# Performance work log

Measured on AMD Instinct MI355X. Metric: run time of the kernel, lower is better.

Reference implementation:

```python
import jax, jax.numpy as jnp
import numpy as np

M, B, N, D, DFF, DCOND = 8, 8, 2048, 512, 2048, 512


def setup_inputs() -> dict:
    key = jax.random.key(0)
    ks = jax.random.split(key, 8)
    s = 0.02  # weight init scale
    return {
        "x": jax.random.normal(ks[0], (B, N, D), dtype=jnp.float32),
        "cond": jax.random.normal(ks[1], (B, DCOND), dtype=jnp.float32),
        "route": jax.random.randint(ks[2], (B,), 0, M, dtype=jnp.int64),
        "W_cond": jax.random.normal(ks[3], (M, DCOND, 2 * D), dtype=jnp.float32) * s,
        "b_cond": jnp.zeros((M, 2 * D), dtype=jnp.float32),
        "W1": jax.random.normal(ks[4], (M, D, DFF), dtype=jnp.float32) * s,
        "b1": jnp.zeros((M, DFF), dtype=jnp.float32),
        "W2": jax.random.normal(ks[5], (M, DFF, D), dtype=jnp.float32) * s,
        "b2": jnp.zeros((M, D), dtype=jnp.float32),
    }


def reference(x, cond, route, W_cond, b_cond, W1, b1, W2, b2):
    # --- all branches computed densely (faithful to the torch module) ---
    # cond modulation per branch: [M, B, 2D]
    mod = jnp.einsum('bc,mcd->mbd', cond, W_cond) + b_cond[:, None, :]
    scale, shift = jnp.split(mod, 2, axis=-1)            # each [M, B, D]
    # FiLM modulate tokens: [M, B, N, D]
    x_mod = x[None] * (1.0 + scale[:, :, None, :]) + shift[:, :, None, :]
    # MLP per branch
    h = jax.nn.gelu(jnp.einsum('mbnd,mdf->mbnf', x_mod, W1) + b1[:, None, None, :])
    stacked = jnp.einsum('mbnf,mfd->mbnd', h, W2) + b2[:, None, None, :]  # [M,B,N,D]
    # --- one-hot select (torch.einsum('mbnd,bm->bnd', stacked, one_hot)) ---
    one_hot = jax.nn.one_hot(route, M, dtype=stacked.dtype)  # [B, M]
    return jnp.einsum('mbnd,bm->bnd', stacked, one_hot)
```

## Files before the change

### kernel.cpp

```cpp
#include <hip/hip_runtime.h>
#include <hip/hip_bf16.h>
#include <cstdint>
#include <cstddef>

#define NEXP   8
#define BATCH  8
#define NTOK   2048
#define DDIM   512
#define DFFDIM 2048
#define DCOND  512

typedef float  f32x4  __attribute__((ext_vector_type(4)));
typedef __bf16 bf16x8 __attribute__((ext_vector_type(8)));

using as1_cvoid = __attribute__((address_space(1))) const void;
using as3_void  = __attribute__((address_space(3))) void;

__device__ __forceinline__ void async_copy16(const void* g, void* l) {
  __builtin_amdgcn_global_load_lds((as1_cvoid*)g, (as3_void*)l, 16, 0, 0);
}

__device__ __forceinline__ unsigned short f2bf_bits(float f) {
  __hip_bfloat16 h = __float2bfloat16(f);
  return *reinterpret_cast<unsigned short*>(&h);
}

__device__ __forceinline__ float gelu_fast(float v) {
  float y = v * fmaf(0.0713548162726f, v * v, 1.5957691216057f);
  float e = exp2f(-1.44269504089f * y);
  return v * __builtin_amdgcn_rcpf(1.0f + e);
}

__global__ void mod_kernel(const float* __restrict__ cond,
                           const int* __restrict__ route,
                           const float* __restrict__ W_cond,
                           const float* __restrict__ b_cond,
                           float* __restrict__ ss) {
  const int b = blockIdx.y;
  const int m = route[b];
  const int tj = threadIdx.x & 63;
  const int cq = threadIdx.x >> 6;
  const int j = blockIdx.x * 64 + tj;
  const float* wc = W_cond + (size_t)m * DCOND * (2 * DDIM);
  const float* cb = cond + (size_t)b * DCOND;
  float acc = 0.f;
#pragma unroll 4
  for (int c = cq * 128; c < cq * 128 + 128; ++c)
    acc += cb[c] * wc[(size_t)c * (2 * DDIM) + j];
  __shared__ float red[4][64];
  red[cq][tj] = acc;
  __syncthreads();
  if (cq == 0) {
    float v = red[0][tj] + red[1][tj] + red[2][tj] + red[3][tj];
    ss[(size_t)b * (2 * DDIM) + j] = v + b_cond[(size_t)m * (2 * DDIM) + j];
  }
}

__global__ void film_kernel(const float* __restrict__ x,
                            const float* __restrict__ ss,
                            __hip_bfloat16* __restrict__ xmod) {
  const size_t idx = (size_t)blockIdx.x * blockDim.x + threadIdx.x;
  const int d4 = (int)(idx & (DDIM / 4 - 1));
  const int b  = (int)(idx >> 18);
  const float4 xv = reinterpret_cast<const float4*>(x)[idx];
  const float4 sc = reinterpret_cast<const float4*>(ss + (size_t)b * 1024)[d4];
  const float4 sh = reinterpret_cast<const float4*>(ss + (size_t)b * 1024 + DDIM)[d4];
  float r0 = xv.x * (1.f + sc.x) + sh.x;
  float r1 = xv.y * (1.f + sc.y) + sh.y;
  float r2 = xv.z * (1.f + sc.z) + sh.z;
  float r3 = xv.w * (1.f + sc.w) + sh.w;
  ushort4 ov;
  ov.x = f2bf_bits(r0); ov.y = f2bf_bits(r1);
  ov.z = f2bf_bits(r2); ov.w = f2bf_bits(r3);
  reinterpret_cast<ushort4*>(xmod)[idx] = ov;
}

__global__ void transpose_cvt(const float* __restrict__ in,
                              __hip_bfloat16* __restrict__ outp,
                              int L, int R,
                              const int* __restrict__ route) {
  const int mi = blockIdx.z;
  bool used = false;
#pragma unroll
  for (int b = 0; b < BATCH; ++b) used |= (route[b] == mi);
  if (!used) return;

  __shared__ float tile[32][33];
  const float* inm = in + (size_t)mi * L * R;
  __hip_bfloat16* outm = outp + (size_t)mi * L * R;
  const int r0 = blockIdx.x * 32, l0 = blockIdx.y * 32;
  const int tx = threadIdx.x, ty = threadIdx.y;
#pragma unroll
  for (int i = 0; i < 32; i += 8)
    tile[ty + i][tx] = inm[(size_t)(l0 + ty + i) * R + r0 + tx];
  __syncthreads();
#pragma unroll
  for (int i = 0; i < 32; i += 8)
    outm[(size_t)(r0 + ty + i) * L + l0 + tx] = __float2bfloat16(tile[tx][ty + i]);
}

template <int EPI>
__global__ __launch_bounds__(512, 1) void gemm_pipe(
    const __hip_bfloat16* __restrict__ Abase,
    const __hip_bfloat16* __restrict__ Btbase,
    const float* __restrict__ biasbase,
    void* __restrict__ outbase,
    const int* __restrict__ route,
    int Mdim, int Ndim, int Kdim, int tilesX) {
  const int bid  = blockIdx.x;
  const int b    = bid & 7;
  const int tile = bid >> 3;
  const int bx   = tile % tilesX;
  const int by   = tile / tilesX;
  const int m = route[b];
  const __hip_bfloat16* A  = Abase  + (size_t)b * Mdim * Kdim;
  const __hip_bfloat16* Bt = Btbase + (size_t)m * Ndim * Kdim;
  const float* bias = biasbase + (size_t)m * Ndim;
  const int r0 = bx * 256;
  const int n0 = by * 128;

  __shared__ alignas(16) __hip_bfloat16 As[2][256 * 64];
  __shared__ alignas(16) __hip_bfloat16 Bs[2][128 * 64];

  const int t = threadIdx.x;
  const int w = t >> 6, l = t & 63;
  const int wm = w >> 2, wn = w & 3;

  const int srow = t >> 3;
  const int scol = (t & 7) ^ ((t >> 3) & 7);

#define STAGE_A(s, k0)                                                        \
  { _Pragma("unroll")                                                         \
    for (int i = 0; i < 4; ++i)                                               \
      async_copy16(A + (size_t)(r0 + i * 64 + srow) * Kdim + (k0) + scol * 8, \
                   &As[s][(i * 512 + w * 64) * 8]); }
#define STAGE_B(s, k0)                                                        \
  { _Pragma("unroll")                                                         \
    for (int i = 0; i < 2; ++i)                                               \
      async_copy16(Bt + (size_t)(n0 + i * 64 + srow) * Kdim + (k0) + scol * 8,\
                   &Bs[s][(i * 512 + w * 64) * 8]); }

  const int lrow = l & 15, lq = l >> 4, lx = l & 7;
  const int abase = (wm * 128 + lrow) * 8;
  const int bbase = (wn * 32 + lrow) * 8;
  const int swz0 = (lq) ^ lx;
  const int swz1 = (4 + lq) ^ lx;

  f32x4 acc[8][2] = {};

  const int nt = Kdim >> 6;

  STAGE_A(0, 0) STAGE_B(0, 0)
  STAGE_A(1, 64) STAGE_B(1, 64)

  for (int kt = 0; kt < nt; ++kt) {
    const int s = kt & 1;
    if (kt + 1 < nt) asm volatile("s_waitcnt vmcnt(6)" ::: "memory");
    else             asm volatile("s_waitcnt vmcnt(0)" ::: "memory");
    __builtin_amdgcn_s_barrier();
    __builtin_amdgcn_sched_barrier(0);

    bf16x8 af[8][2], bfr[2][2];
#pragma unroll
    for (int mb = 0; mb < 8; ++mb) {
      af[mb][0] = *reinterpret_cast<const bf16x8*>(&As[s][(abase + mb * 128 + swz0) * 8]);
      af[mb][1] = *reinterpret_cast<const bf16x8*>(&As[s][(abase + mb * 128 + swz1) * 8]);
    }
#pragma unroll
    for (int nb = 0; nb < 2; ++nb) {
      bfr[nb][0] = *reinterpret_cast<const bf16x8*>(&Bs[s][(bbase + nb * 128 + swz0) * 8]);
      bfr[nb][1] = *reinterpret_cast<const bf16x8*>(&Bs[s][(bbase + nb * 128 + swz1) * 8]);
    }
    asm volatile("s_waitcnt lgkmcnt(0)" ::: "memory");
    __builtin_amdgcn_sched_barrier(0);
    __builtin_amdgcn_s_barrier();
    __builtin_amdgcn_sched_barrier(0);

    if (kt + 2 < nt) { STAGE_A(s, (kt + 2) * 64) STAGE_B(s, (kt + 2) * 64) }

    __builtin_amdgcn_s_setprio(1);
#pragma unroll
    for (int mb = 0; mb < 8; ++mb)
#pragma unroll
      for (int nb = 0; nb < 2; ++nb) {
        acc[mb][nb] = __builtin_amdgcn_mfma_f32_16x16x32_bf16(
            af[mb][0], bfr[nb][0], acc[mb][nb], 0, 0, 0);
        acc[mb][nb] = __builtin_amdgcn_mfma_f32_16x16x32_bf16(
            af[mb][1], bfr[nb][1], acc[mb][nb], 0, 0, 0);
      }
    __builtin_amdgcn_s_setprio(0);
  }
#undef STAGE_A
#undef STAGE_B

  if (EPI == 0) {
    __hip_bfloat16* out = (__hip_bfloat16*)outbase + (size_t)b * Mdim * Ndim;
#pragma unroll
    for (int mb = 0; mb < 8; ++mb) {
      const int row = r0 + wm * 128 + mb * 16 + lq * 4;
#pragma unroll
      for (int nb = 0; nb < 2; ++nb) {
        const int col = n0 + wn * 32 + nb * 16 + lrow;
        const float bv = bias[col];
#pragma unroll
        for (int j = 0; j < 4; ++j) {
          float g = gelu_fast(acc[mb][nb][j] + bv);
          out[(size_t)(row + j) * Ndim + col] = __float2bfloat16(g);
        }
      }
    }
  } else {
    float* out = (float*)outbase + (size_t)b * Mdim * Ndim;
#pragma unroll
    for (int mb = 0; mb < 8; ++mb) {
      const int row = r0 + wm * 128 + mb * 16 + lq * 4;
#pragma unroll
      for (int nb = 0; nb < 2; ++nb) {
        const int col = n0 + wn * 32 + nb * 16 + lrow;
        const float bv = bias[col];
#pragma unroll
        for (int j = 0; j < 4; ++j)
          out[(size_t)(row + j) * Ndim + col] = acc[mb][nb][j] + bv;
      }
    }
  }
}

extern "C" void kernel_launch(void* const* d_in, const int* in_sizes, int n_in,
                              void* d_out, int out_size, void* d_ws, size_t ws_size,
                              hipStream_t stream) {
  const float* x      = (const float*)d_in[0];
  const float* cond   = (const float*)d_in[1];
  const int*   route  = (const int*)d_in[2];
  const float* W_cond = (const float*)d_in[3];
  const float* b_cond = (const float*)d_in[4];
  const float* W1     = (const float*)d_in[5];
  const float* b1     = (const float*)d_in[6];
  const float* W2     = (const float*)d_in[7];
  const float* b2     = (const float*)d_in[8];
  float* out = (float*)d_out;

  const size_t SS_OFF   = 0;
  const size_t XMOD_OFF = 32768;
  const size_t W1T_OFF  = XMOD_OFF + (size_t)BATCH * NTOK * DDIM * 2;
  const size_t W2T_OFF  = W1T_OFF + (size_t)NEXP * DDIM * DFFDIM * 2;
  const size_t H_OFF    = W2T_OFF + (size_t)NEXP * DFFDIM * DDIM * 2;
  const size_t NEED     = H_OFF + (size_t)BATCH * NTOK * DFFDIM * 2;
  if (ws_size < NEED) return;

  char* ws = (char*)d_ws;
  float* ss            = (float*)(ws + SS_OFF);
  __hip_bfloat16* xmod = (__hip_bfloat16*)(ws + XMOD_OFF);
  __hip_bfloat16* w1t  = (__hip_bfloat16*)(ws + W1T_OFF);
  __hip_bfloat16* w2t  = (__hip_bfloat16*)(ws + W2T_OFF);
  __hip_bfloat16* h    = (__hip_bfloat16*)(ws + H_OFF);

  mod_kernel<<<dim3(2 * DDIM / 64, BATCH), 256, 0, stream>>>(cond, route, W_cond, b_cond, ss);

  {
    const size_t groups = (size_t)BATCH * NTOK * DDIM / 4;
    film_kernel<<<(unsigned)(groups / 256), 256, 0, stream>>>(x, ss, xmod);
  }

  transpose_cvt<<<dim3(DFFDIM / 32, DDIM / 32, NEXP), dim3(32, 8), 0, stream>>>(W1, w1t, DDIM, DFFDIM, route);
  transpose_cvt<<<dim3(DDIM / 32, DFFDIM / 32, NEXP), dim3(32, 8), 0, stream>>>(W2, w2t, DFFDIM, DDIM, route);

  gemm_pipe<0><<<(NTOK / 256) * (DFFDIM / 128) * BATCH, 512, 0, stream>>>(
      xmod, w1t, b1, h, route, NTOK, DFFDIM, DDIM, NTOK / 256);

  gemm_pipe<1><<<(NTOK / 256) * (DDIM / 128) * BATCH, 512, 0, stream>>>(
      h, w2t, b2, out, route, NTOK, DDIM, DFFDIM, NTOK / 256);
}
```

Before: 146.2 us.

## Triple-buffer GEMM LDS stages and drop the mid-iteration barrier

Grows the LDS ring for the A and B tiles in both GEMMs from two stages to three. The prefetch for stage k+2 now goes out right after the top-of-loop barrier, before the LDS fragment reads, so the second per-iteration barrier and the explicit lgkmcnt wait are no longer needed. The s_setprio hints around the MFMA block are also removed. This costs more LDS per block (about 144KB), which still fits with one block per CU, and relies on the three-slot rotation to keep writes from overlapping reads.

```diff
diff --git a/kernel.cpp b/kernel.cpp
--- a/kernel.cpp
+++ b/kernel.cpp
@@ -100,7 +100,7 @@
 }
 
 template <int EPI>
-__global__ __launch_bounds__(512, 1) void gemm_pipe(
+__global__ __launch_bounds__(512, 1) void gemm_pipe3(
     const __hip_bfloat16* __restrict__ Abase,
     const __hip_bfloat16* __restrict__ Btbase,
     const float* __restrict__ biasbase,
@@ -119,8 +119,8 @@
   const int r0 = bx * 256;
   const int n0 = by * 128;
 
-  __shared__ alignas(16) __hip_bfloat16 As[2][256 * 64];
-  __shared__ alignas(16) __hip_bfloat16 Bs[2][128 * 64];
+  __shared__ alignas(16) __hip_bfloat16 As[3][256 * 64];
+  __shared__ alignas(16) __hip_bfloat16 Bs[3][128 * 64];
 
   const int t = threadIdx.x;
   const int w = t >> 6, l = t & 63;
@@ -129,16 +129,15 @@
   const int srow = t >> 3;
   const int scol = (t & 7) ^ ((t >> 3) & 7);
 
-#define STAGE_A(s, k0)                                                        \
+#define STAGE(s_, k0)                                                         \
   { _Pragma("unroll")                                                         \
     for (int i = 0; i < 4; ++i)                                               \
       async_copy16(A + (size_t)(r0 + i * 64 + srow) * Kdim + (k0) + scol * 8, \
-                   &As[s][(i * 512 + w * 64) * 8]); }
-#define STAGE_B(s, k0)                                                        \
-  { _Pragma("unroll")                                                         \
+                   &As[s_][(i * 512 + w * 64) * 8]);                          \
+    _Pragma("unroll")                                                         \
     for (int i = 0; i < 2; ++i)                                               \
       async_copy16(Bt + (size_t)(n0 + i * 64 + srow) * Kdim + (k0) + scol * 8,\
-                   &Bs[s][(i * 512 + w * 64) * 8]); }
+                   &Bs[s_][(i * 512 + w * 64) * 8]); }
 
   const int lrow = l & 15, lq = l >> 4, lx = l & 7;
   const int abase = (wm * 128 + lrow) * 8;
@@ -147,38 +146,34 @@
   const int swz1 = (4 + lq) ^ lx;
 
   f32x4 acc[8][2] = {};
-
   const int nt = Kdim >> 6;
 
-  STAGE_A(0, 0) STAGE_B(0, 0)
-  STAGE_A(1, 64) STAGE_B(1, 64)
-
+  STAGE(0, 0)
+  STAGE(1, 64)
+
+  int s = 0;
   for (int kt = 0; kt < nt; ++kt) {
-    const int s = kt & 1;
     if (kt + 1 < nt) asm volatile("s_waitcnt vmcnt(6)" ::: "memory");
     else             asm volatile("s_waitcnt vmcnt(0)" ::: "memory");
     __builtin_amdgcn_s_barrier();
     __builtin_amdgcn_sched_barrier(0);
 
+    int s2 = s + 2; if (s2 >= 3) s2 -= 3;
+    if (kt + 2 < nt) STAGE(s2, (kt + 2) * 64)
+
+    const __hip_bfloat16* as_ = As[s];
+    const __hip_bfloat16* bs_ = Bs[s];
     bf16x8 af[8][2], bfr[2][2];
 #pragma unroll
+    for (int nb = 0; nb < 2; ++nb) {
+      bfr[nb][0] = *reinterpret_cast<const bf16x8*>(&bs_[(bbase + nb * 128 + swz0) * 8]);
+      bfr[nb][1] = *reinterpret_cast<const bf16x8*>(&bs_[(bbase + nb * 128 + swz1) * 8]);
+    }
+#pragma unroll
     for (int mb = 0; mb < 8; ++mb) {
-      af[mb][0] = *reinterpret_cast<const bf16x8*>(&As[s][(abase + mb * 128 + swz0) * 8]);
-      af[mb][1] = *reinterpret_cast<const bf16x8*>(&As[s][(abase + mb * 128 + swz1) * 8]);
-    }
-#pragma unroll
-    for (int nb = 0; nb < 2; ++nb) {
-      bfr[nb][0] = *reinterpret_cast<const bf16x8*>(&Bs[s][(bbase + nb * 128 + swz0) * 8]);
-      bfr[nb][1] = *reinterpret_cast<const bf16x8*>(&Bs[s][(bbase + nb * 128 + swz1) * 8]);
-    }
-    asm volatile("s_waitcnt lgkmcnt(0)" ::: "memory");
-    __builtin_amdgcn_sched_barrier(0);
-    __builtin_amdgcn_s_barrier();
-    __builtin_amdgcn_sched_barrier(0);
-
-    if (kt + 2 < nt) { STAGE_A(s, (kt + 2) * 64) STAGE_B(s, (kt + 2) * 64) }
-
-    __builtin_amdgcn_s_setprio(1);
+      af[mb][0] = *reinterpret_cast<const bf16x8*>(&as_[(abase + mb * 128 + swz0) * 8]);
+      af[mb][1] = *reinterpret_cast<const bf16x8*>(&as_[(abase + mb * 128 + swz1) * 8]);
+    }
 #pragma unroll
     for (int mb = 0; mb < 8; ++mb)
 #pragma unroll
@@ -188,10 +183,10 @@
         acc[mb][nb] = __builtin_amdgcn_mfma_f32_16x16x32_bf16(
             af[mb][1], bfr[nb][1], acc[mb][nb], 0, 0, 0);
       }
-    __builtin_amdgcn_s_setprio(0);
-  }
-#undef STAGE_A
-#undef STAGE_B
+
+    ++s; if (s == 3) s = 0;
+  }
+#undef STAGE
 
   if (EPI == 0) {
     __hip_bfloat16* out = (__hip_bfloat16*)outbase + (size_t)b * Mdim * Ndim;
@@ -265,9 +260,9 @@
   transpose_cvt<<<dim3(DFFDIM / 32, DDIM / 32, NEXP), dim3(32, 8), 0, stream>>>(W1, w1t, DDIM, DFFDIM, route);
   transpose_cvt<<<dim3(DDIM / 32, DFFDIM / 32, NEXP), dim3(32, 8), 0, stream>>>(W2, w2t, DFFDIM, DDIM, route);
 
-  gemm_pipe<0><<<(NTOK / 256) * (DFFDIM / 128) * BATCH, 512, 0, stream>>>(
+  gemm_pipe3<0><<<(NTOK / 256) * (DFFDIM / 128) * BATCH, 512, 0, stream>>>(
       xmod, w1t, b1, h, route, NTOK, DFFDIM, DDIM, NTOK / 256);
 
-  gemm_pipe<1><<<(NTOK / 256) * (DDIM / 128) * BATCH, 512, 0, stream>>>(
+  gemm_pipe3<1><<<(NTOK / 256) * (DDIM / 128) * BATCH, 512, 0, stream>>>(
       h, w2t, b2, out, route, NTOK, DDIM, DFFDIM, NTOK / 256);
 }
```

New measurement: 152.3 us. 1.04x slower.
